# Performance work log

Hardware: AMD Instinct MI355X
Metric: run time of the kernel (lower is better)

## Reference

```python
import jax, jax.numpy as jnp
import numpy as np

B, H, W, C = 128, 256, 1024, 1
N_HOLES = 5
PROB = 1.0
HOLE_MINW, HOLE_MAXW = W // 10, int(W / 2.5)   # 102, 409
HOLE_MINH, HOLE_MAXH = H // 10, int(H / 2.5)   # 25, 102


def setup_inputs() -> dict:
    key = jax.random.key(0)
    k0, k1, k2, k3, k4, k5 = jax.random.split(key, 6)
    x = jax.random.normal(k0, (B, H, W, C), dtype=jnp.float32)
    # hole centers: tf.random.uniform((bsz,n), 0, dim-1, int32) -> [0, dim-1)
    xs = jax.random.randint(k1, (B, N_HOLES), 0, W - 1, dtype=jnp.int32)
    ys = jax.random.randint(k2, (B, N_HOLES), 0, H - 1, dtype=jnp.int32)
    # hole sizes: raw in [0, max-min); reference adds the min offset
    xs_w_raw = jax.random.randint(k3, (B, N_HOLES), 0, HOLE_MAXW - HOLE_MINW, dtype=jnp.int32)
    ys_h_raw = jax.random.randint(k4, (B, N_HOLES), 0, HOLE_MAXH - HOLE_MINH, dtype=jnp.int32)
    # per-hole activation uniforms (hole active iff act_rand < PROB)
    act_rand = jax.random.uniform(k5, (B, N_HOLES), dtype=jnp.float32)
    return {"x": x, "xs": xs, "ys": ys, "xs_w_raw": xs_w_raw,
            "ys_h_raw": ys_h_raw, "act_rand": act_rand}


def _build_mask(xs, ys, xs_w_raw, ys_h_raw, act_rand):
    xs_w = xs_w_raw + HOLE_MINW                      # (B, N) hole widths
    ys_h = ys_h_raw + HOLE_MINH                      # (B, N) hole heights
    xs_start = jnp.clip(xs - xs_w // 2, 0, W - 2)
    xs_end   = jnp.clip(xs + xs_w // 2, 1, W - 1)
    ys_start = jnp.clip(ys - ys_h // 2, 0, H - 2)
    ys_end   = jnp.clip(ys + ys_h // 2, 1, H - 1)
    act = act_rand < PROB                            # (B, N) hole-wise activation
    idx_h = jnp.arange(H)
    idx_w = jnp.arange(W)
    mask = jnp.zeros((B, H, W), dtype=bool)
    for n in range(N_HOLES):                         # small fixed hole count
        mh = (ys_start[:, n, None] <= idx_h) & (idx_h <= ys_end[:, n, None])  # (B, H)
        mw = (xs_start[:, n, None] <= idx_w) & (idx_w <= xs_end[:, n, None])  # (B, W)
        m = mh[:, :, None] & mw[:, None, :]                                   # (B, H, W)
        mask = mask | (m & act[:, n, None, None])
    return mask


def reference(x, xs, ys, xs_w_raw, ys_h_raw, act_rand):
    mask = _build_mask(xs, ys, xs_w_raw, ys_h_raw, act_rand)   # (B, H, W) bool
    maskf = mask[..., None].astype(x.dtype)                    # (B, H, W, 1)
    fill = jnp.mean(x)  # hole_fill='min' path: hf = ones * reduce_mean(x)
    return x * (1.0 - maskf) + maskf * fill
```

## Files before the change

kernel.cpp:

```cpp
#include <hip/hip_runtime.h>


#define BB 128
#define HH 256
#define WW 1024
#define N_HOLES 5
#define HOLE_MINW (WW / 10)
#define HOLE_MINH (HH / 10)
#define N_ELEM (BB * HH * WW)
#define RED_BLOCKS 2048

__global__ __launch_bounds__(256) void reduce_kernel(
    const float* __restrict__ x, float* __restrict__ partials) {
  int tid = blockIdx.x * blockDim.x + threadIdx.x;
  int stride = gridDim.x * blockDim.x;
  const float4* x4 = (const float4*)x;
  const int n4 = N_ELEM / 4;
  float s = 0.0f;
  for (int i = tid; i < n4; i += stride) {
    float4 v = x4[i];
    s += (v.x + v.y) + (v.z + v.w);
  }
  #pragma unroll
  for (int off = 32; off > 0; off >>= 1) s += __shfl_down(s, off, 64);
  __shared__ float wsum[4];
  int lane = threadIdx.x & 63;
  int wave = threadIdx.x >> 6;
  if (lane == 0) wsum[wave] = s;
  __syncthreads();
  if (threadIdx.x == 0)
    partials[blockIdx.x] = (wsum[0] + wsum[1]) + (wsum[2] + wsum[3]);
}

__global__ __launch_bounds__(256) void finalize_kernel(
    const float* __restrict__ partials, float* __restrict__ mean_out) {
  float s = 0.0f;
  for (int i = threadIdx.x; i < RED_BLOCKS; i += 256) s += partials[i];
  #pragma unroll
  for (int off = 32; off > 0; off >>= 1) s += __shfl_down(s, off, 64);
  __shared__ float wsum[4];
  int lane = threadIdx.x & 63;
  int wave = threadIdx.x >> 6;
  if (lane == 0) wsum[wave] = s;
  __syncthreads();
  if (threadIdx.x == 0) {
    float t = (wsum[0] + wsum[1]) + (wsum[2] + wsum[3]);
    mean_out[0] = t * (1.0f / (float)N_ELEM);
  }
}

__global__ __launch_bounds__(256) void apply_kernel(
    const float* __restrict__ x,
    const int* __restrict__ xs, const int* __restrict__ ys,
    const int* __restrict__ xs_w_raw, const int* __restrict__ ys_h_raw,
    const float* __restrict__ act_rand,
    const float* __restrict__ mean_ptr,
    float* __restrict__ out) {
  int row = blockIdx.x;
  int b = row >> 8;
  int h = row & 255;

  float mean = mean_ptr[0];

  int lo[N_HOLES], hi[N_HOLES];
  #pragma unroll
  for (int n = 0; n < N_HOLES; ++n) {
    int base = b * N_HOLES + n;
    int cx = xs[base];
    int cy = ys[base];
    int hw = (xs_w_raw[base] + HOLE_MINW) >> 1;
    int hh = (ys_h_raw[base] + HOLE_MINH) >> 1;
    int ys_s = min(max(cy - hh, 0), HH - 2);
    int ys_e = min(max(cy + hh, 1), HH - 1);
    bool act = act_rand[base] < 1.0f;
    bool in_row = act && (ys_s <= h) && (h <= ys_e);
    int xs_s = min(max(cx - hw, 0), WW - 2);
    int xs_e = min(max(cx + hw, 1), WW - 1);
    lo[n] = in_row ? xs_s : 1;
    hi[n] = in_row ? xs_e : 0;
  }

  int w0 = (int)threadIdx.x * 4;
  long idx = (long)row * WW + w0;
  float4 v = *(const float4*)(x + idx);
  float r[4] = {v.x, v.y, v.z, v.w};
  #pragma unroll
  for (int j = 0; j < 4; ++j) {
    int w = w0 + j;
    bool m = false;
    #pragma unroll
    for (int n = 0; n < N_HOLES; ++n)
      m = m || ((lo[n] <= w) && (w <= hi[n]));
    if (m) r[j] = mean;
  }
  float4 o;
  o.x = r[0]; o.y = r[1]; o.z = r[2]; o.w = r[3];
  *(float4*)(out + idx) = o;
}

extern "C" void kernel_launch(void* const* d_in, const int* in_sizes, int n_in,
                              void* d_out, int out_size, void* d_ws, size_t ws_size,
                              hipStream_t stream) {
  const float* x        = (const float*)d_in[0];
  const int* xs         = (const int*)d_in[1];
  const int* ys         = (const int*)d_in[2];
  const int* xs_w_raw   = (const int*)d_in[3];
  const int* ys_h_raw   = (const int*)d_in[4];
  const float* act_rand = (const float*)d_in[5];
  float* out = (float*)d_out;

  float* partials = (float*)d_ws;
  float* mean_ptr = partials + RED_BLOCKS;

  reduce_kernel<<<RED_BLOCKS, 256, 0, stream>>>(x, partials);
  finalize_kernel<<<1, 256, 0, stream>>>(partials, mean_ptr);
  apply_kernel<<<BB * HH, 256, 0, stream>>>(x, xs, ys, xs_w_raw, ys_h_raw,
                                            act_rand, mean_ptr, out);
}
```

Baseline: 268.5 us.

## Fuse mean reduction with copy, then scatter-fill only hole rectangles

The reduction pass now also copies x to the output using nontemporal loads and stores. A second kernel recomputes the mean from partials in every block and writes the mean only into each active hole's rectangle. This drops the second full read of x and the per-element mask test. In exchange, overlapping holes get written redundantly and every block re-sums the partials.

```diff
diff --git a/kernel.cpp b/kernel.cpp
--- a/kernel.cpp
+++ b/kernel.cpp
@@ -9,16 +9,23 @@
 #define HOLE_MINH (HH / 10)
 #define N_ELEM (BB * HH * WW)
 #define RED_BLOCKS 2048
+#define MAXSPAN 104
+#define VROWS (BB * N_HOLES * MAXSPAN)
 
-__global__ __launch_bounds__(256) void reduce_kernel(
-    const float* __restrict__ x, float* __restrict__ partials) {
+typedef float f4v __attribute__((ext_vector_type(4)));
+
+__global__ __launch_bounds__(256) void copyreduce_kernel(
+    const float* __restrict__ x, float* __restrict__ out,
+    float* __restrict__ partials) {
   int tid = blockIdx.x * blockDim.x + threadIdx.x;
   int stride = gridDim.x * blockDim.x;
-  const float4* x4 = (const float4*)x;
+  const f4v* x4 = (const f4v*)x;
+  f4v* out4 = (f4v*)out;
   const int n4 = N_ELEM / 4;
   float s = 0.0f;
   for (int i = tid; i < n4; i += stride) {
-    float4 v = x4[i];
+    f4v v = __builtin_nontemporal_load(&x4[i]);
+    __builtin_nontemporal_store(v, &out4[i]);
     s += (v.x + v.y) + (v.z + v.w);
   }
   #pragma unroll
@@ -32,70 +39,55 @@
     partials[blockIdx.x] = (wsum[0] + wsum[1]) + (wsum[2] + wsum[3]);
 }
 
-__global__ __launch_bounds__(256) void finalize_kernel(
-    const float* __restrict__ partials, float* __restrict__ mean_out) {
+__global__ __launch_bounds__(256) void holefill_kernel(
+    const int* __restrict__ xs, const int* __restrict__ ys,
+    const int* __restrict__ xs_w_raw, const int* __restrict__ ys_h_raw,
+    const float* __restrict__ act_rand,
+    const float* __restrict__ partials,
+    float* __restrict__ out) {
   float s = 0.0f;
   for (int i = threadIdx.x; i < RED_BLOCKS; i += 256) s += partials[i];
   #pragma unroll
   for (int off = 32; off > 0; off >>= 1) s += __shfl_down(s, off, 64);
   __shared__ float wsum[4];
+  __shared__ float smean;
   int lane = threadIdx.x & 63;
   int wave = threadIdx.x >> 6;
   if (lane == 0) wsum[wave] = s;
   __syncthreads();
   if (threadIdx.x == 0) {
     float t = (wsum[0] + wsum[1]) + (wsum[2] + wsum[3]);
-    mean_out[0] = t * (1.0f / (float)N_ELEM);
+    smean = t * (1.0f / (float)N_ELEM);
   }
-}
+  __syncthreads();
+  float mean = smean;
 
-__global__ __launch_bounds__(256) void apply_kernel(
-    const float* __restrict__ x,
-    const int* __restrict__ xs, const int* __restrict__ ys,
-    const int* __restrict__ xs_w_raw, const int* __restrict__ ys_h_raw,
-    const float* __restrict__ act_rand,
-    const float* __restrict__ mean_ptr,
-    float* __restrict__ out) {
-  int row = blockIdx.x;
-  int b = row >> 8;
-  int h = row & 255;
+  for (int v = blockIdx.x; v < VROWS; v += gridDim.x) {
+    int b = v / (N_HOLES * MAXSPAN);
+    int rem = v - b * (N_HOLES * MAXSPAN);
+    int n = rem / MAXSPAN;
+    int r = rem - n * MAXSPAN;
+    int base = b * N_HOLES + n;
 
-  float mean = mean_ptr[0];
-
-  int lo[N_HOLES], hi[N_HOLES];
-  #pragma unroll
-  for (int n = 0; n < N_HOLES; ++n) {
-    int base = b * N_HOLES + n;
     int cx = xs[base];
     int cy = ys[base];
     int hw = (xs_w_raw[base] + HOLE_MINW) >> 1;
     int hh = (ys_h_raw[base] + HOLE_MINH) >> 1;
     int ys_s = min(max(cy - hh, 0), HH - 2);
     int ys_e = min(max(cy + hh, 1), HH - 1);
-    bool act = act_rand[base] < 1.0f;
-    bool in_row = act && (ys_s <= h) && (h <= ys_e);
     int xs_s = min(max(cx - hw, 0), WW - 2);
     int xs_e = min(max(cx + hw, 1), WW - 1);
-    lo[n] = in_row ? xs_s : 1;
-    hi[n] = in_row ? xs_e : 0;
+    bool act = act_rand[base] < 1.0f;
+
+    int h = ys_s + r;
+    if (!act || h > ys_e) continue;
+
+    long rowbase = ((long)b * HH + h) * WW;
+    int w = xs_s + (int)threadIdx.x;
+    if (w <= xs_e) out[rowbase + w] = mean;
+    w += 256;
+    if (w <= xs_e) out[rowbase + w] = mean;
   }
-
-  int w0 = (int)threadIdx.x * 4;
-  long idx = (long)row * WW + w0;
-  float4 v = *(const float4*)(x + idx);
-  float r[4] = {v.x, v.y, v.z, v.w};
-  #pragma unroll
-  for (int j = 0; j < 4; ++j) {
-    int w = w0 + j;
-    bool m = false;
-    #pragma unroll
-    for (int n = 0; n < N_HOLES; ++n)
-      m = m || ((lo[n] <= w) && (w <= hi[n]));
-    if (m) r[j] = mean;
-  }
-  float4 o;
-  o.x = r[0]; o.y = r[1]; o.z = r[2]; o.w = r[3];
-  *(float4*)(out + idx) = o;
 }
 
 extern "C" void kernel_launch(void* const* d_in, const int* in_sizes, int n_in,
@@ -108,12 +100,9 @@
   const int* ys_h_raw   = (const int*)d_in[4];
   const float* act_rand = (const float*)d_in[5];
   float* out = (float*)d_out;
+  float* partials = (float*)d_ws;
 
-  float* partials = (float*)d_ws;
-  float* mean_ptr = partials + RED_BLOCKS;
-
-  reduce_kernel<<<RED_BLOCKS, 256, 0, stream>>>(x, partials);
-  finalize_kernel<<<1, 256, 0, stream>>>(partials, mean_ptr);
-  apply_kernel<<<BB * HH, 256, 0, stream>>>(x, xs, ys, xs_w_raw, ys_h_raw,
-                                            act_rand, mean_ptr, out);
+  copyreduce_kernel<<<RED_BLOCKS, 256, 0, stream>>>(x, out, partials);
+  holefill_kernel<<<RED_BLOCKS, 256, 0, stream>>>(xs, ys, xs_w_raw, ys_h_raw,
+                                                  act_rand, partials, out);
 }
```

New measurement: 275.3 us. +2.6%, slower.
